# Performance work log

Measured on AMD Instinct MI355X. Metric: run time of the kernel, lower is better.

The kernel has to match this reference:

```python
import jax, jax.numpy as jnp
import numpy as np

B, U, V = 4, 64, 256
IN_DIM, STATE_DIM, CODE_DIM = 768, 768, 384
NUM_HEADS, HEAD_DIM = 8, 64
INNER = NUM_HEADS * HEAD_DIM  # 512
SCALE = HEAD_DIM ** 0.5


def _ln(x, g, b, eps=1e-5):
    mu = jnp.mean(x, axis=-1, keepdims=True)
    var = jnp.var(x, axis=-1, keepdims=True)
    return (x - mu) * jax.lax.rsqrt(var + eps) * g + b


def setup_inputs() -> dict:
    key = jax.random.key(0)
    ks = jax.random.split(key, 12)
    def w(k, shape, s=0.02):
        return jax.random.normal(k, shape, jnp.float32) * s
    return {
        "receiver_states": jax.random.normal(ks[0], (B, U, STATE_DIM), jnp.float32),
        "receiver_codes": jax.random.normal(ks[1], (B, U, CODE_DIM), jnp.float32),
        "sender_states": jax.random.normal(ks[2], (B, V, IN_DIM), jnp.float32),
        "ln_r_g": jnp.ones((STATE_DIM,), jnp.float32),
        "ln_r_b": jnp.zeros((STATE_DIM,), jnp.float32),
        "ln_s_g": jnp.ones((IN_DIM,), jnp.float32),
        "ln_s_b": jnp.zeros((IN_DIM,), jnp.float32),
        "Wq": w(ks[3], (STATE_DIM, INNER)), "bq": jnp.zeros((INNER,), jnp.float32), "Wmq": w(ks[4], (CODE_DIM, STATE_DIM)),
        "Wk": w(ks[5], (IN_DIM, INNER)),   "bk": jnp.zeros((INNER,), jnp.float32), "Wmk": w(ks[6], (CODE_DIM, IN_DIM)),
        "Wv": w(ks[7], (IN_DIM, INNER)),   "bv": jnp.zeros((INNER,), jnp.float32), "Wmv": w(ks[8], (CODE_DIM, IN_DIM)),
        "We": w(ks[9], (INNER, STATE_DIM)), "be": jnp.zeros((STATE_DIM,), jnp.float32), "Wme": w(ks[10], (CODE_DIM, INNER)),
        "gamma": jnp.ones((STATE_DIM,), jnp.float32),  # LayerScale, init 1.0
    }


def reference(receiver_states, receiver_codes, sender_states,
              ln_r_g, ln_r_b, ln_s_g, ln_s_b,
              Wq, bq, Wmq, Wk, bk, Wmk, Wv, bv, Wmv, We, be, Wme, gamma):
    r = _ln(receiver_states, ln_r_g, ln_r_b)   # (b,u,ds)
    s = _ln(sender_states, ln_s_g, ln_s_b)     # (b,v,di)
    # ModFC: y = (x * (1 + ctx @ Wm)) @ W + b  (code-conditioned input modulation)
    q = (r * (1.0 + receiver_codes @ Wmq)) @ Wq + bq          # (b,u,inner)
    mk = 1.0 + receiver_codes @ Wmk                           # (b,u,di)
    mv = 1.0 + receiver_codes @ Wmv                           # (b,u,di)
    xs = s[:, :, None, :]                                     # (b,v,1,di)
    k = (xs * mk[:, None, :, :]) @ Wk + bk                    # (b,v,u,inner)
    v = (xs * mv[:, None, :, :]) @ Wv + bv                    # (b,v,u,inner)
    qh = q.reshape(B, U, NUM_HEADS, HEAD_DIM)
    kh = k.reshape(B, V, U, NUM_HEADS, HEAD_DIM)
    vh = v.reshape(B, V, U, NUM_HEADS, HEAD_DIM)
    scores = jnp.einsum('buhc,bvuhc->bhuv', qh, kh) / SCALE   # (b,h,u,v)
    weights = jax.nn.softmax(scores, axis=-1)
    msg = jnp.einsum('bhuv,bvuhc->buhc', weights, vh).reshape(B, U, INNER)
    out = (msg * (1.0 + receiver_codes @ Wme)) @ We + be      # exit ModFC -> (b,u,ds)
    out = out * gamma                                         # LayerScale
    return receiver_states + out                              # residual
```

## Files before the change

kernel.cpp:

```cpp
#include <hip/hip_runtime.h>


#define DD 768
#define CDIM 384
#define NH 8
#define HD 64
#define INNER 512
#define VV 256

__device__ __forceinline__ void fma4(float4& a, float s, const float4& b) {
  a.x += s * b.x; a.y += s * b.y; a.z += s * b.z; a.w += s * b.w;
}

template <int K, int NS>
__device__ __forceinline__ void gcore(const float* __restrict__ A0, int lda,
                                      const float* __restrict__ Bp,
                                      float4& a0, float4& a1, float4& a2,
                                      float4& a3) {
  float4 b0[8], b1[8];
#pragma unroll
  for (int i = 0; i < 8; i++) b0[i] = *(const float4*)(Bp + (size_t)i * NS);
  const float* Bq = Bp + (size_t)8 * NS;
#pragma unroll 1
  for (int kk = 0; kk < K; kk += 16) {
#pragma unroll
    for (int i = 0; i < 8; i++) b1[i] = *(const float4*)(Bq + (size_t)i * NS);
    Bq += (size_t)8 * NS;
#pragma unroll
    for (int i = 0; i < 8; i++) {
      float4 bv = b0[i]; int k = kk + i;
      fma4(a0, A0[k], bv); fma4(a1, A0[lda + k], bv);
      fma4(a2, A0[2 * lda + k], bv); fma4(a3, A0[3 * lda + k], bv);
    }
    if (kk + 16 < K) {
#pragma unroll
      for (int i = 0; i < 8; i++) b0[i] = *(const float4*)(Bq + (size_t)i * NS);
      Bq += (size_t)8 * NS;
    }
#pragma unroll
    for (int i = 0; i < 8; i++) {
      float4 bv = b1[i]; int k = kk + 8 + i;
      fma4(a0, A0[k], bv); fma4(a1, A0[lda + k], bv);
      fma4(a2, A0[2 * lda + k], bv); fma4(a3, A0[3 * lda + k], bv);
    }
  }
}

__global__ __launch_bounds__(256, 2) void k_s1(
    const float* __restrict__ ss, const float* __restrict__ rs,
    const float* __restrict__ g_s, const float* __restrict__ b_s,
    const float* __restrict__ g_r, const float* __restrict__ b_r,
    const float* __restrict__ codes, const float* __restrict__ Wmq,
    const float* __restrict__ Wmk, const float* __restrict__ Wmv,
    const float* __restrict__ Wme, const float* __restrict__ Wk,
    float* __restrict__ s_ln, float* __restrict__ r_ln,
    float* __restrict__ cp, float* __restrict__ WkT) {
  __shared__ float SB[6144];
  int bid = blockIdx.x, t = threadIdx.x;
  if (bid < 176) {
    int nc = bid % 11, mb = bid / 11;
    int base = nc * 256;
    const float* W; int N, colW;
    if (base < 768)       { W = Wmq; N = DD;    colW = base; }
    else if (base < 1536) { W = Wmk; N = DD;    colW = base - 768; }
    else if (base < 2304) { W = Wmv; N = DD;    colW = base - 1536; }
    else                  { W = Wme; N = INNER; colW = base - 2304; }
    int m0 = mb * 16;
#pragma unroll
    for (int p = 0; p < 24; p++) {
      int idx = p * 256 + t, r = idx / 384, k = idx % 384;
      SB[idx] = codes[(size_t)(m0 + r) * CDIM + k];
    }
    __syncthreads();
    int kl = t & 63, wid = t >> 6;
    const float* A0 = SB + (wid * 4) * 384;
    float4 a0 = {0,0,0,0}, a1 = {0,0,0,0}, a2 = {0,0,0,0}, a3 = {0,0,0,0};
    if (N == DD)
      gcore<384, DD>(A0, 384, W + colW + 4 * kl, a0, a1, a2, a3);
    else
      gcore<384, INNER>(A0, 384, W + colW + 4 * kl, a0, a1, a2, a3);
    int m = m0 + wid * 4, gcol = base + 4 * kl;
    *(float4*)(cp + (size_t)m * 2816 + gcol) = a0;
    *(float4*)(cp + (size_t)(m + 1) * 2816 + gcol) = a1;
    *(float4*)(cp + (size_t)(m + 2) * 2816 + gcol) = a2;
    *(float4*)(cp + (size_t)(m + 3) * 2816 + gcol) = a3;
  } else if (bid < 272) {
    int tid = bid - 176;
    int d0 = (tid >> 3) * 64, c0 = (tid & 7) * 64;
    int j = t & 63, i0 = t >> 6;
#pragma unroll
    for (int p = 0; p < 16; p++) {
      int i = p * 4 + i0;
      SB[i * 65 + j] = Wk[(size_t)(d0 + i) * INNER + c0 + j];
    }
    __syncthreads();
#pragma unroll
    for (int p = 0; p < 16; p++) {
      int i = p * 4 + i0;
      WkT[(size_t)(c0 + i) * DD + d0 + j] = SB[j * 65 + i];
    }
  } else {
    int rr = bid - 272;
    const float *x, *g, *bb; float* y; int r;
    if (rr < 1024) { x = ss; g = g_s; bb = b_s; y = s_ln; r = rr; }
    else           { x = rs; g = g_r; bb = b_r; y = r_ln; r = rr - 1024; }
    const float* xr = x + (size_t)r * DD;
    float v0 = xr[t], v1 = xr[t + 256], v2 = xr[t + 512];
    float s = v0 + v1 + v2, sq = v0 * v0 + v1 * v1 + v2 * v2;
    for (int o = 32; o > 0; o >>= 1) {
      s += __shfl_down(s, o, 64); sq += __shfl_down(sq, o, 64);
    }
    int wid = t >> 6, lane = t & 63;
    if (lane == 0) { SB[wid] = s; SB[wid + 4] = sq; }
    __syncthreads();
    float sum = SB[0] + SB[1] + SB[2] + SB[3];
    float ssq = SB[4] + SB[5] + SB[6] + SB[7];
    float mu = sum * (1.0f / 768.0f);
    float var = ssq * (1.0f / 768.0f) - mu * mu;
    float rstd = rsqrtf(var + 1e-5f);
    float* yr = y + (size_t)r * DD;
    yr[t]       = (v0 - mu) * rstd * g[t]       + bb[t];
    yr[t + 256] = (v1 - mu) * rstd * g[t + 256] + bb[t + 256];
    yr[t + 512] = (v2 - mu) * rstd * g[t + 512] + bb[t + 512];
  }
}

__global__ __launch_bounds__(256, 2) void k_s2(
    const float* __restrict__ s_ln, const float* __restrict__ r_ln,
    const float* __restrict__ cp, const float* __restrict__ Wq,
    float* __restrict__ sT, float* __restrict__ qp) {
  __shared__ float SB[4160];
  int bid = blockIdx.x, t = threadIdx.x;
  if (bid < 128) {
    int ks = bid & 3, tile = bid >> 2, nc = tile & 1, mb = tile >> 1;
    int m0 = mb * 16, col0 = nc * 256, k0 = ks * 192;
#pragma unroll
    for (int p = 0; p < 12; p++) {
      int idx = p * 256 + t, r = idx / 192, k = idx % 192;
      int d = k0 + k;
      float mqv = cp[(size_t)(m0 + r) * 2816 + d] + 1.0f;
      SB[idx] = r_ln[(size_t)(m0 + r) * DD + d] * mqv;
    }
    __syncthreads();
    int kl = t & 63, wid = t >> 6;
    int col = col0 + 4 * kl;
    const float* A0 = SB + (wid * 4) * 192;
    float4 a0 = {0,0,0,0}, a1 = {0,0,0,0}, a2 = {0,0,0,0}, a3 = {0,0,0,0};
    gcore<192, INNER>(A0, 192, Wq + (size_t)k0 * INNER + col, a0, a1, a2, a3);
    int m = m0 + wid * 4;
    float* dst = qp + (size_t)ks * (256 * INNER);
    *(float4*)(dst + (size_t)m * INNER + col) = a0;
    *(float4*)(dst + (size_t)(m + 1) * INNER + col) = a1;
    *(float4*)(dst + (size_t)(m + 2) * INNER + col) = a2;
    *(float4*)(dst + (size_t)(m + 3) * INNER + col) = a3;
  } else {
    int tid = bid - 128;
    int vt = tid & 3, dt = (tid >> 2) % 12, b = tid / 48;
    int v0 = vt * 64, d0 = dt * 64;
    int j = t & 63, i0 = t >> 6;
#pragma unroll
    for (int p = 0; p < 16; p++) {
      int i = p * 4 + i0;
      SB[i * 65 + j] = s_ln[(size_t)(b * VV + v0 + i) * DD + d0 + j];
    }
    __syncthreads();
#pragma unroll
    for (int p = 0; p < 16; p++) {
      int i = p * 4 + i0;
      sT[((size_t)b * DD + d0 + i) * VV + v0 + j] = SB[j * 65 + i];
    }
  }
}

__global__ __launch_bounds__(256, 2) void k_s3(
    const float* __restrict__ qp, const float* __restrict__ bq,
    const float* __restrict__ WkT, const float* __restrict__ cp,
    const float* __restrict__ bk, float* __restrict__ qm,
    float* __restrict__ qbk) {
  __shared__ float SB[1024];
  int bid = blockIdx.x, t = threadIdx.x;
  if (bid < 384) {
    int h = bid & 7, dc = (bid >> 3) % 3, mb = bid / 24;
    int m0 = mb * 16;
#pragma unroll
    for (int p = 0; p < 4; p++) {
      int idx = p * 256 + t, r = idx >> 6, c = idx & 63;
      int i = h * HD + c;
      size_t off = (size_t)(m0 + r) * INNER + i;
      SB[idx] = qp[off] + qp[131072 + off] + qp[262144 + off] +
                qp[393216 + off] + bq[i];
    }
    __syncthreads();
    int kl = t & 63, wid = t >> 6;
    int col = dc * 256 + 4 * kl;
    const float* A0 = SB + (wid * 4) * HD;
    float4 a0 = {0,0,0,0}, a1 = {0,0,0,0}, a2 = {0,0,0,0}, a3 = {0,0,0,0};
    gcore<64, DD>(A0, HD, WkT + (size_t)(h * HD) * DD + col, a0, a1, a2, a3);
#pragma unroll
    for (int j = 0; j < 4; j++) {
      float4 a = (j == 0) ? a0 : (j == 1) ? a1 : (j == 2) ? a2 : a3;
      int m = m0 + wid * 4 + j;
      const float* mkp = cp + (size_t)m * 2816 + 768 + col;
      float4 o = {a.x * (mkp[0] + 1.0f), a.y * (mkp[1] + 1.0f),
                  a.z * (mkp[2] + 1.0f), a.w * (mkp[3] + 1.0f)};
      *(float4*)(qm + ((size_t)m * NH + h) * DD + col) = o;
    }
  } else {
    int m = bid - 384;
    size_t off = (size_t)m * INNER;
    SB[t] = (qp[off + t] + qp[131072 + off + t] + qp[262144 + off + t] +
             qp[393216 + off + t] + bq[t]) * bk[t];
    int t2 = t + 256;
    SB[t2] = (qp[off + t2] + qp[131072 + off + t2] + qp[262144 + off + t2] +
              qp[393216 + off + t2] + bq[t2]) * bk[t2];
    __syncthreads();
    if (t < 8) {
      float a = 0.f;
      for (int c = 0; c < HD; c++) a += SB[t * HD + c];
      qbk[m * NH + t] = a;
    }
  }
}

__global__ __launch_bounds__(256, 2) void k_s4(
    const float* __restrict__ qm, const float* __restrict__ sT,
    float* __restrict__ scp) {
  __shared__ float SB[3072];
  int bid = blockIdx.x, t = threadIdx.x;
  int ks = bid & 3, b = (bid >> 2) & 3, mb = bid >> 4;
  int gi0 = b * 512 + mb * 16, k0 = ks * 192;
#pragma unroll
  for (int p = 0; p < 12; p++) {
    int idx = p * 256 + t, r = idx / 192, k = idx % 192;
    SB[idx] = qm[(size_t)(gi0 + r) * DD + k0 + k];
  }
  __syncthreads();
  int kl = t & 63, wid = t >> 6;
  int col = 4 * kl;
  const float* A0 = SB + (wid * 4) * 192;
  float4 a0 = {0,0,0,0}, a1 = {0,0,0,0}, a2 = {0,0,0,0}, a3 = {0,0,0,0};
  gcore<192, VV>(A0, 192, sT + ((size_t)b * DD + k0) * VV + col, a0, a1, a2, a3);
  int gi = gi0 + wid * 4;
  float* dst = scp + (size_t)ks * (2048 * VV);
  *(float4*)(dst + (size_t)gi * VV + col) = a0;
  *(float4*)(dst + (size_t)(gi + 1) * VV + col) = a1;
  *(float4*)(dst + (size_t)(gi + 2) * VV + col) = a2;
  *(float4*)(dst + (size_t)(gi + 3) * VV + col) = a3;
}

__global__ __launch_bounds__(256, 2) void k_s5(
    const float* __restrict__ scp, const float* __restrict__ qbk,
    const float* __restrict__ s_ln, const float* __restrict__ cp,
    float* __restrict__ wsm) {
  __shared__ float SC[4096];
  int bid = blockIdx.x, t = threadIdx.x;
  int dc = bid % 3, up = (bid / 3) % 32, b = bid / 96;
  int gi0 = b * 512 + up * 16;
#pragma unroll
  for (int p = 0; p < 16; p++) {
    int idx = p * 256 + t, r = idx >> 8, c = idx & 255;
    size_t o = (size_t)(gi0 + r) * VV + c;
    float v = scp[o] + scp[524288 + o] + scp[1048576 + o] + scp[1572864 + o];
    int m = b * 64 + up * 2 + (r >> 3), h = r & 7;
    SC[idx] = (v + qbk[m * NH + h]) * 0.125f;
  }
  __syncthreads();
  int wid = t >> 6, lane = t & 63;
#pragma unroll
  for (int j = 0; j < 4; j++) {
    int r = wid * 4 + j;
    float x0 = SC[r * 256 + lane],       x1 = SC[r * 256 + lane + 64];
    float x2 = SC[r * 256 + lane + 128], x3 = SC[r * 256 + lane + 192];
    float mx = fmaxf(fmaxf(x0, x1), fmaxf(x2, x3));
    for (int o = 1; o < 64; o <<= 1) mx = fmaxf(mx, __shfl_xor(mx, o, 64));
    float e0 = __expf(x0 - mx), e1 = __expf(x1 - mx);
    float e2 = __expf(x2 - mx), e3 = __expf(x3 - mx);
    float sm = e0 + e1 + e2 + e3;
    for (int o = 1; o < 64; o <<= 1) sm += __shfl_xor(sm, o, 64);
    float rinv = 1.0f / sm;
    SC[r * 256 + lane] = e0 * rinv;       SC[r * 256 + lane + 64] = e1 * rinv;
    SC[r * 256 + lane + 128] = e2 * rinv; SC[r * 256 + lane + 192] = e3 * rinv;
  }
  __syncthreads();
  int kl = t & 63;
  int col = dc * 256 + 4 * kl;
  const float* A0 = SC + (wid * 4) * 256;
  float4 a0 = {0,0,0,0}, a1 = {0,0,0,0}, a2 = {0,0,0,0}, a3 = {0,0,0,0};
  gcore<VV, DD>(A0, 256, s_ln + (size_t)(b * VV) * DD + col, a0, a1, a2, a3);
#pragma unroll
  for (int j = 0; j < 4; j++) {
    float4 a = (j == 0) ? a0 : (j == 1) ? a1 : (j == 2) ? a2 : a3;
    int r = wid * 4 + j;
    int ul = r >> 3, h = r & 7, m = b * 64 + up * 2 + ul;
    const float* mvp = cp + (size_t)m * 2816 + 1536 + col;
    float4 o = {a.x * (mvp[0] + 1.0f), a.y * (mvp[1] + 1.0f),
                a.z * (mvp[2] + 1.0f), a.w * (mvp[3] + 1.0f)};
    *(float4*)(wsm + ((size_t)h * 256 + m) * DD + col) = o;
  }
}

__global__ __launch_bounds__(256, 2) void k_s6(
    const float* __restrict__ wsm, const float* __restrict__ Wv,
    float* __restrict__ mmp) {
  __shared__ float AL[6144];
  int bid = blockIdx.x, t = threadIdx.x;
  int hp = bid & 1, ks = (bid >> 1) & 7, mb = bid >> 4;
  int h0 = hp * 4, m0 = mb * 16, k0 = ks * 96;
#pragma unroll
  for (int p = 0; p < 24; p++) {
    int idx = p * 256 + t;
    int e = idx / 1536, rem = idx % 1536, r = rem / 96, k = rem % 96;
    AL[idx] = wsm[((size_t)(h0 + e) * 256 + m0 + r) * DD + k0 + k];
  }
  __syncthreads();
  int kl = t & 63, wid = t >> 6;
  int hs = kl >> 4, c4 = 4 * (kl & 15);
  int colg = h0 * HD + hs * HD + c4;
  const float* A0 = AL + (hs * 16 + wid * 4) * 96;
  float4 a0 = {0,0,0,0}, a1 = {0,0,0,0}, a2 = {0,0,0,0}, a3 = {0,0,0,0};
  gcore<96, INNER>(A0, 96, Wv + (size_t)k0 * INNER + colg, a0, a1, a2, a3);
  float* dst = mmp + (size_t)ks * (256 * INNER);
  int m = m0 + wid * 4;
  *(float4*)(dst + (size_t)m * INNER + colg) = a0;
  *(float4*)(dst + (size_t)(m + 1) * INNER + colg) = a1;
  *(float4*)(dst + (size_t)(m + 2) * INNER + colg) = a2;
  *(float4*)(dst + (size_t)(m + 3) * INNER + colg) = a3;
}

__global__ __launch_bounds__(256, 2) void k_s7(
    const float* __restrict__ mmp, const float* __restrict__ bvv,
    const float* __restrict__ cp, const float* __restrict__ We,
    float* __restrict__ op) {
  __shared__ float AL[1024];
  int bid = blockIdx.x, t = threadIdx.x;
  int ks = bid & 7, dc = (bid >> 3) % 3, mb = bid / 24;
  int m0 = mb * 16, k0 = ks * 64;
#pragma unroll
  for (int p = 0; p < 4; p++) {
    int idx = p * 256 + t, r = idx >> 6, k = idx & 63;
    int i = k0 + k;
    size_t off = (size_t)(m0 + r) * INNER + i;
    float v = mmp[off] + mmp[131072 + off] + mmp[262144 + off] +
              mmp[393216 + off] + mmp[524288 + off] + mmp[655360 + off] +
              mmp[786432 + off] + mmp[917504 + off];
    float mev = cp[(size_t)(m0 + r) * 2816 + 2304 + i] + 1.0f;
    AL[idx] = (v + bvv[i]) * mev;
  }
  __syncthreads();
  int kl = t & 63, wid = t >> 6;
  int col = dc * 256 + 4 * kl;
  const float* A0 = AL + (wid * 4) * 64;
  float4 a0 = {0,0,0,0}, a1 = {0,0,0,0}, a2 = {0,0,0,0}, a3 = {0,0,0,0};
  gcore<64, DD>(A0, 64, We + (size_t)k0 * DD + col, a0, a1, a2, a3);
  float* dst = op + (size_t)ks * (256 * DD);
  int m = m0 + wid * 4;
  *(float4*)(dst + (size_t)m * DD + col) = a0;
  *(float4*)(dst + (size_t)(m + 1) * DD + col) = a1;
  *(float4*)(dst + (size_t)(m + 2) * DD + col) = a2;
  *(float4*)(dst + (size_t)(m + 3) * DD + col) = a3;
}

__global__ __launch_bounds__(256) void k_s8(
    const float* __restrict__ op, const float* __restrict__ be,
    const float* __restrict__ gamma, const float* __restrict__ rs,
    float* __restrict__ outp) {
  int m = blockIdx.x, t = threadIdx.x;
#pragma unroll
  for (int j = 0; j < 3; j++) {
    int d = t + j * 256;
    size_t off = (size_t)m * DD + d;
    float v = op[off] + op[196608 + off] + op[393216 + off] +
              op[589824 + off] + op[786432 + off] + op[983040 + off] +
              op[1179648 + off] + op[1376256 + off];
    outp[off] = rs[off] + (v + be[d]) * gamma[d];
  }
}

extern "C" void kernel_launch(void* const* d_in, const int* in_sizes, int n_in,
                              void* d_out, int out_size, void* d_ws, size_t ws_size,
                              hipStream_t stream) {
  const float* rs     = (const float*)d_in[0];
  const float* codes  = (const float*)d_in[1];
  const float* ss     = (const float*)d_in[2];
  const float* ln_r_g = (const float*)d_in[3];
  const float* ln_r_b = (const float*)d_in[4];
  const float* ln_s_g = (const float*)d_in[5];
  const float* ln_s_b = (const float*)d_in[6];
  const float* Wq  = (const float*)d_in[7];
  const float* bq  = (const float*)d_in[8];
  const float* Wk  = (const float*)d_in[10];
  const float* bk  = (const float*)d_in[11];
  const float* Wmq = (const float*)d_in[9];
  const float* Wmk = (const float*)d_in[12];
  const float* Wv  = (const float*)d_in[13];
  const float* bv  = (const float*)d_in[14];
  const float* Wmv = (const float*)d_in[15];
  const float* We  = (const float*)d_in[16];
  const float* be  = (const float*)d_in[17];
  const float* Wme = (const float*)d_in[18];
  const float* gamma = (const float*)d_in[19];

  float* w = (float*)d_ws;
  float* s_ln = w;
  float* r_ln = w + 786432;
  float* WkT  = w + 983040;
  float* qp   = w + 1376256;
  float* sT   = w + 1900544;
  float* cp   = w + 2686976;
  float* qbk  = w + 3407872;
  float* qm   = w + 3409920;
  float* scp  = w + 4982784;
  float* wsm  = qm;
  float* mmp  = r_ln;
  float* op   = scp;

  k_s1<<<dim3(1552), 256, 0, stream>>>(ss, rs, ln_s_g, ln_s_b, ln_r_g, ln_r_b,
                                       codes, Wmq, Wmk, Wmv, Wme, Wk,
                                       s_ln, r_ln, cp, WkT);
  k_s2<<<dim3(320), 256, 0, stream>>>(s_ln, r_ln, cp, Wq, sT, qp);
  k_s3<<<dim3(640), 256, 0, stream>>>(qp, bq, WkT, cp, bk, qm, qbk);
  k_s4<<<dim3(512), 256, 0, stream>>>(qm, sT, scp);
  k_s5<<<dim3(384), 256, 0, stream>>>(scp, qbk, s_ln, cp, wsm);
  k_s6<<<dim3(256), 256, 0, stream>>>(wsm, Wv, mmp);
  k_s7<<<dim3(384), 256, 0, stream>>>(mmp, bv, cp, We, op);
  k_s8<<<dim3(256), 256, 0, stream>>>(op, be, gamma, rs, (float*)d_out);
}
```

Measured before the change: 198.2 us.

## Fuse eight stage kernels into one persistent kernel with grid barriers

```diff
diff --git a/kernel.cpp b/kernel.cpp
--- a/kernel.cpp
+++ b/kernel.cpp
@@ -7,6 +7,7 @@
 #define HD 64
 #define INNER 512
 #define VV 256
+#define GRID 448
 
 __device__ __forceinline__ void fma4(float4& a, float s, const float4& b) {
   a.x += s * b.x; a.y += s * b.y; a.z += s * b.z; a.w += s * b.w;
@@ -46,333 +47,346 @@
   }
 }
 
-__global__ __launch_bounds__(256, 2) void k_s1(
-    const float* __restrict__ ss, const float* __restrict__ rs,
-    const float* __restrict__ g_s, const float* __restrict__ b_s,
-    const float* __restrict__ g_r, const float* __restrict__ b_r,
-    const float* __restrict__ codes, const float* __restrict__ Wmq,
-    const float* __restrict__ Wmk, const float* __restrict__ Wmv,
-    const float* __restrict__ Wme, const float* __restrict__ Wk,
-    float* __restrict__ s_ln, float* __restrict__ r_ln,
-    float* __restrict__ cp, float* __restrict__ WkT) {
+__device__ __forceinline__ void gbar(unsigned* bar, unsigned target) {
+  __syncthreads();
+  if (threadIdx.x == 0) {
+    __threadfence();
+    atomicAdd(bar, 1u);
+    while (atomicAdd(bar, 0u) < target) __builtin_amdgcn_s_sleep(2);
+    __threadfence();
+  }
+  __syncthreads();
+}
+
+__global__ __launch_bounds__(256, 2) void k_all(
+    const float* __restrict__ rs, const float* __restrict__ codes,
+    const float* __restrict__ ss, const float* __restrict__ g_r,
+    const float* __restrict__ b_r, const float* __restrict__ g_s,
+    const float* __restrict__ b_s, const float* __restrict__ Wq,
+    const float* __restrict__ bq, const float* __restrict__ Wmq,
+    const float* __restrict__ Wk, const float* __restrict__ bk,
+    const float* __restrict__ Wmk, const float* __restrict__ Wv,
+    const float* __restrict__ bvv, const float* __restrict__ Wmv,
+    const float* __restrict__ We, const float* __restrict__ be,
+    const float* __restrict__ Wme, const float* __restrict__ gamma,
+    float* __restrict__ w, float* __restrict__ outp, unsigned* __restrict__ bar) {
   __shared__ float SB[6144];
-  int bid = blockIdx.x, t = threadIdx.x;
-  if (bid < 176) {
-    int nc = bid % 11, mb = bid / 11;
-    int base = nc * 256;
-    const float* W; int N, colW;
-    if (base < 768)       { W = Wmq; N = DD;    colW = base; }
-    else if (base < 1536) { W = Wmk; N = DD;    colW = base - 768; }
-    else if (base < 2304) { W = Wmv; N = DD;    colW = base - 1536; }
-    else                  { W = Wme; N = INNER; colW = base - 2304; }
-    int m0 = mb * 16;
-#pragma unroll
-    for (int p = 0; p < 24; p++) {
-      int idx = p * 256 + t, r = idx / 384, k = idx % 384;
-      SB[idx] = codes[(size_t)(m0 + r) * CDIM + k];
-    }
-    __syncthreads();
-    int kl = t & 63, wid = t >> 6;
-    const float* A0 = SB + (wid * 4) * 384;
-    float4 a0 = {0,0,0,0}, a1 = {0,0,0,0}, a2 = {0,0,0,0}, a3 = {0,0,0,0};
-    if (N == DD)
-      gcore<384, DD>(A0, 384, W + colW + 4 * kl, a0, a1, a2, a3);
-    else
-      gcore<384, INNER>(A0, 384, W + colW + 4 * kl, a0, a1, a2, a3);
-    int m = m0 + wid * 4, gcol = base + 4 * kl;
-    *(float4*)(cp + (size_t)m * 2816 + gcol) = a0;
-    *(float4*)(cp + (size_t)(m + 1) * 2816 + gcol) = a1;
-    *(float4*)(cp + (size_t)(m + 2) * 2816 + gcol) = a2;
-    *(float4*)(cp + (size_t)(m + 3) * 2816 + gcol) = a3;
-  } else if (bid < 272) {
-    int tid = bid - 176;
-    int d0 = (tid >> 3) * 64, c0 = (tid & 7) * 64;
-    int j = t & 63, i0 = t >> 6;
-#pragma unroll
-    for (int p = 0; p < 16; p++) {
-      int i = p * 4 + i0;
-      SB[i * 65 + j] = Wk[(size_t)(d0 + i) * INNER + c0 + j];
-    }
-    __syncthreads();
-#pragma unroll
-    for (int p = 0; p < 16; p++) {
-      int i = p * 4 + i0;
-      WkT[(size_t)(c0 + i) * DD + d0 + j] = SB[j * 65 + i];
-    }
-  } else {
-    int rr = bid - 272;
-    const float *x, *g, *bb; float* y; int r;
-    if (rr < 1024) { x = ss; g = g_s; bb = b_s; y = s_ln; r = rr; }
-    else           { x = rs; g = g_r; bb = b_r; y = r_ln; r = rr - 1024; }
-    const float* xr = x + (size_t)r * DD;
-    float v0 = xr[t], v1 = xr[t + 256], v2 = xr[t + 512];
-    float s = v0 + v1 + v2, sq = v0 * v0 + v1 * v1 + v2 * v2;
-    for (int o = 32; o > 0; o >>= 1) {
-      s += __shfl_down(s, o, 64); sq += __shfl_down(sq, o, 64);
-    }
-    int wid = t >> 6, lane = t & 63;
-    if (lane == 0) { SB[wid] = s; SB[wid + 4] = sq; }
-    __syncthreads();
-    float sum = SB[0] + SB[1] + SB[2] + SB[3];
-    float ssq = SB[4] + SB[5] + SB[6] + SB[7];
-    float mu = sum * (1.0f / 768.0f);
-    float var = ssq * (1.0f / 768.0f) - mu * mu;
-    float rstd = rsqrtf(var + 1e-5f);
-    float* yr = y + (size_t)r * DD;
-    yr[t]       = (v0 - mu) * rstd * g[t]       + bb[t];
-    yr[t + 256] = (v1 - mu) * rstd * g[t + 256] + bb[t + 256];
-    yr[t + 512] = (v2 - mu) * rstd * g[t + 512] + bb[t + 512];
-  }
-}
-
-__global__ __launch_bounds__(256, 2) void k_s2(
-    const float* __restrict__ s_ln, const float* __restrict__ r_ln,
-    const float* __restrict__ cp, const float* __restrict__ Wq,
-    float* __restrict__ sT, float* __restrict__ qp) {
-  __shared__ float SB[4160];
-  int bid = blockIdx.x, t = threadIdx.x;
-  if (bid < 128) {
-    int ks = bid & 3, tile = bid >> 2, nc = tile & 1, mb = tile >> 1;
-    int m0 = mb * 16, col0 = nc * 256, k0 = ks * 192;
+  float* s_ln = w;
+  float* r_ln = w + 786432;
+  float* WkT  = w + 983040;
+  float* qp   = w + 1376256;
+  float* sT   = w + 1900544;
+  float* cp   = w + 2686976;
+  float* qbk  = w + 3407872;
+  float* qm   = w + 3409920;
+  float* scp  = w + 4982784;
+  float* wsm  = qm;
+  float* mmp  = r_ln;
+  float* op   = scp;
+
+  int t = threadIdx.x;
+  unsigned target = 0;
+
+  for (int tile = blockIdx.x; tile < 1552; tile += GRID) {
+    if (tile < 176) {
+      int nc = tile % 11, mb = tile / 11;
+      int base = nc * 256;
+      const float* W; int N, colW;
+      if (base < 768)       { W = Wmq; N = DD;    colW = base; }
+      else if (base < 1536) { W = Wmk; N = DD;    colW = base - 768; }
+      else if (base < 2304) { W = Wmv; N = DD;    colW = base - 1536; }
+      else                  { W = Wme; N = INNER; colW = base - 2304; }
+      int m0 = mb * 16;
+#pragma unroll
+      for (int p = 0; p < 24; p++) {
+        int idx = p * 256 + t, r = idx / 384, k = idx % 384;
+        SB[idx] = codes[(size_t)(m0 + r) * CDIM + k];
+      }
+      __syncthreads();
+      int kl = t & 63, wid = t >> 6;
+      const float* A0 = SB + (wid * 4) * 384;
+      float4 a0 = {0,0,0,0}, a1 = {0,0,0,0}, a2 = {0,0,0,0}, a3 = {0,0,0,0};
+      if (N == DD)
+        gcore<384, DD>(A0, 384, W + colW + 4 * kl, a0, a1, a2, a3);
+      else
+        gcore<384, INNER>(A0, 384, W + colW + 4 * kl, a0, a1, a2, a3);
+      int m = m0 + wid * 4, gcol = base + 4 * kl;
+      *(float4*)(cp + (size_t)m * 2816 + gcol) = a0;
+      *(float4*)(cp + (size_t)(m + 1) * 2816 + gcol) = a1;
+      *(float4*)(cp + (size_t)(m + 2) * 2816 + gcol) = a2;
+      *(float4*)(cp + (size_t)(m + 3) * 2816 + gcol) = a3;
+    } else if (tile < 272) {
+      int tid = tile - 176;
+      int d0 = (tid >> 3) * 64, c0 = (tid & 7) * 64;
+      int j = t & 63, i0 = t >> 6;
+#pragma unroll
+      for (int p = 0; p < 16; p++) {
+        int i = p * 4 + i0;
+        SB[i * 65 + j] = Wk[(size_t)(d0 + i) * INNER + c0 + j];
+      }
+      __syncthreads();
+#pragma unroll
+      for (int p = 0; p < 16; p++) {
+        int i = p * 4 + i0;
+        WkT[(size_t)(c0 + i) * DD + d0 + j] = SB[j * 65 + i];
+      }
+    } else {
+      int rr = tile - 272;
+      const float *x, *g, *bb; float* y; int r;
+      if (rr < 1024) { x = ss; g = g_s; bb = b_s; y = s_ln; r = rr; }
+      else           { x = rs; g = g_r; bb = b_r; y = r_ln; r = rr - 1024; }
+      const float* xr = x + (size_t)r * DD;
+      float v0 = xr[t], v1 = xr[t + 256], v2 = xr[t + 512];
+      float s = v0 + v1 + v2, sq = v0 * v0 + v1 * v1 + v2 * v2;
+      for (int o = 32; o > 0; o >>= 1) {
+        s += __shfl_down(s, o, 64); sq += __shfl_down(sq, o, 64);
+      }
+      int wid = t >> 6, lane = t & 63;
+      if (lane == 0) { SB[wid] = s; SB[wid + 4] = sq; }
+      __syncthreads();
+      float sum = SB[0] + SB[1] + SB[2] + SB[3];
+      float ssq = SB[4] + SB[5] + SB[6] + SB[7];
+      float mu = sum * (1.0f / 768.0f);
+      float var = ssq * (1.0f / 768.0f) - mu * mu;
+      float rstd = rsqrtf(var + 1e-5f);
+      float* yr = y + (size_t)r * DD;
+      yr[t]       = (v0 - mu) * rstd * g[t]       + bb[t];
+      yr[t + 256] = (v1 - mu) * rstd * g[t + 256] + bb[t + 256];
+      yr[t + 512] = (v2 - mu) * rstd * g[t + 512] + bb[t + 512];
+    }
+    __syncthreads();
+  }
+  target += GRID; gbar(bar, target);
+
+  for (int tile = blockIdx.x; tile < 320; tile += GRID) {
+    if (tile < 128) {
+      int ks = tile & 3, t2 = tile >> 2, nc = t2 & 1, mb = t2 >> 1;
+      int m0 = mb * 16, col0 = nc * 256, k0 = ks * 192;
+#pragma unroll
+      for (int p = 0; p < 12; p++) {
+        int idx = p * 256 + t, r = idx / 192, k = idx % 192;
+        int d = k0 + k;
+        float mqv = cp[(size_t)(m0 + r) * 2816 + d] + 1.0f;
+        SB[idx] = r_ln[(size_t)(m0 + r) * DD + d] * mqv;
+      }
+      __syncthreads();
+      int kl = t & 63, wid = t >> 6;
+      int col = col0 + 4 * kl;
+      const float* A0 = SB + (wid * 4) * 192;
+      float4 a0 = {0,0,0,0}, a1 = {0,0,0,0}, a2 = {0,0,0,0}, a3 = {0,0,0,0};
+      gcore<192, INNER>(A0, 192, Wq + (size_t)k0 * INNER + col, a0, a1, a2, a3);
+      int m = m0 + wid * 4;
+      float* dst = qp + (size_t)ks * (256 * INNER);
+      *(float4*)(dst + (size_t)m * INNER + col) = a0;
+      *(float4*)(dst + (size_t)(m + 1) * INNER + col) = a1;
+      *(float4*)(dst + (size_t)(m + 2) * INNER + col) = a2;
+      *(float4*)(dst + (size_t)(m + 3) * INNER + col) = a3;
+    } else {
+      int tid = tile - 128;
+      int vt = tid & 3, dt = (tid >> 2) % 12, b = tid / 48;
+      int v0 = vt * 64, d0 = dt * 64;
+      int j = t & 63, i0 = t >> 6;
+#pragma unroll
+      for (int p = 0; p < 16; p++) {
+        int i = p * 4 + i0;
+        SB[i * 65 + j] = s_ln[(size_t)(b * VV + v0 + i) * DD + d0 + j];
+      }
+      __syncthreads();
+#pragma unroll
+      for (int p = 0; p < 16; p++) {
+        int i = p * 4 + i0;
+        sT[((size_t)b * DD + d0 + i) * VV + v0 + j] = SB[j * 65 + i];
+      }
+    }
+    __syncthreads();
+  }
+  target += GRID; gbar(bar, target);
+
+  for (int tile = blockIdx.x; tile < 640; tile += GRID) {
+    if (tile < 384) {
+      int h = tile & 7, dc = (tile >> 3) % 3, mb = tile / 24;
+      int m0 = mb * 16;
+#pragma unroll
+      for (int p = 0; p < 4; p++) {
+        int idx = p * 256 + t, r = idx >> 6, c = idx & 63;
+        int i = h * HD + c;
+        size_t off = (size_t)(m0 + r) * INNER + i;
+        SB[idx] = qp[off] + qp[131072 + off] + qp[262144 + off] +
+                  qp[393216 + off] + bq[i];
+      }
+      __syncthreads();
+      int kl = t & 63, wid = t >> 6;
+      int col = dc * 256 + 4 * kl;
+      const float* A0 = SB + (wid * 4) * HD;
+      float4 a0 = {0,0,0,0}, a1 = {0,0,0,0}, a2 = {0,0,0,0}, a3 = {0,0,0,0};
+      gcore<64, DD>(A0, HD, WkT + (size_t)(h * HD) * DD + col, a0, a1, a2, a3);
+#pragma unroll
+      for (int j = 0; j < 4; j++) {
+        float4 a = (j == 0) ? a0 : (j == 1) ? a1 : (j == 2) ? a2 : a3;
+        int m = m0 + wid * 4 + j;
+        const float* mkp = cp + (size_t)m * 2816 + 768 + col;
+        float4 o = {a.x * (mkp[0] + 1.0f), a.y * (mkp[1] + 1.0f),
+                    a.z * (mkp[2] + 1.0f), a.w * (mkp[3] + 1.0f)};
+        *(float4*)(qm + ((size_t)m * NH + h) * DD + col) = o;
+      }
+    } else {
+      int m = tile - 384;
+      size_t off = (size_t)m * INNER;
+      SB[t] = (qp[off + t] + qp[131072 + off + t] + qp[262144 + off + t] +
+               qp[393216 + off + t] + bq[t]) * bk[t];
+      int t2 = t + 256;
+      SB[t2] = (qp[off + t2] + qp[131072 + off + t2] + qp[262144 + off + t2] +
+                qp[393216 + off + t2] + bq[t2]) * bk[t2];
+      __syncthreads();
+      if (t < 8) {
+        float a = 0.f;
+        for (int c = 0; c < HD; c++) a += SB[t * HD + c];
+        qbk[m * NH + t] = a;
+      }
+    }
+    __syncthreads();
+  }
+  target += GRID; gbar(bar, target);
+
+  for (int tile = blockIdx.x; tile < 512; tile += GRID) {
+    int ks = tile & 3, b = (tile >> 2) & 3, mb = tile >> 4;
+    int gi0 = b * 512 + mb * 16, k0 = ks * 192;
 #pragma unroll
     for (int p = 0; p < 12; p++) {
       int idx = p * 256 + t, r = idx / 192, k = idx % 192;
-      int d = k0 + k;
-      float mqv = cp[(size_t)(m0 + r) * 2816 + d] + 1.0f;
-      SB[idx] = r_ln[(size_t)(m0 + r) * DD + d] * mqv;
+      SB[idx] = qm[(size_t)(gi0 + r) * DD + k0 + k];
     }
     __syncthreads();
     int kl = t & 63, wid = t >> 6;
-    int col = col0 + 4 * kl;
+    int col = 4 * kl;
     const float* A0 = SB + (wid * 4) * 192;
     float4 a0 = {0,0,0,0}, a1 = {0,0,0,0}, a2 = {0,0,0,0}, a3 = {0,0,0,0};
-    gcore<192, INNER>(A0, 192, Wq + (size_t)k0 * INNER + col, a0, a1, a2, a3);
+    gcore<192, VV>(A0, 192, sT + ((size_t)b * DD + k0) * VV + col, a0, a1, a2, a3);
+    int gi = gi0 + wid * 4;
+    float* dst = scp + (size_t)ks * (2048 * VV);
+    *(float4*)(dst + (size_t)gi * VV + col) = a0;
+    *(float4*)(dst + (size_t)(gi + 1) * VV + col) = a1;
+    *(float4*)(dst + (size_t)(gi + 2) * VV + col) = a2;
+    *(float4*)(dst + (size_t)(gi + 3) * VV + col) = a3;
+    __syncthreads();
+  }
+  target += GRID; gbar(bar, target);
+
+  for (int tile = blockIdx.x; tile < 384; tile += GRID) {
+    int dc = tile % 3, up = (tile / 3) % 32, b = tile / 96;
+    int gi0 = b * 512 + up * 16;
+#pragma unroll
+    for (int p = 0; p < 16; p++) {
+      int idx = p * 256 + t, r = idx >> 8, c = idx & 255;
+      size_t o = (size_t)(gi0 + r) * VV + c;
+      float v = scp[o] + scp[524288 + o] + scp[1048576 + o] + scp[1572864 + o];
+      int m = b * 64 + up * 2 + (r >> 3), h = r & 7;
+      SB[idx] = (v + qbk[m * NH + h]) * 0.125f;
+    }
+    __syncthreads();
+    int wid = t >> 6, lane = t & 63;
+#pragma unroll
+    for (int j = 0; j < 4; j++) {
+      int r = wid * 4 + j;
+      float x0 = SB[r * 256 + lane],       x1 = SB[r * 256 + lane + 64];
+      float x2 = SB[r * 256 + lane + 128], x3 = SB[r * 256 + lane + 192];
+      float mx = fmaxf(fmaxf(x0, x1), fmaxf(x2, x3));
+      for (int o = 1; o < 64; o <<= 1) mx = fmaxf(mx, __shfl_xor(mx, o, 64));
+      float e0 = __expf(x0 - mx), e1 = __expf(x1 - mx);
+      float e2 = __expf(x2 - mx), e3 = __expf(x3 - mx);
+      float sm = e0 + e1 + e2 + e3;
+      for (int o = 1; o < 64; o <<= 1) sm += __shfl_xor(sm, o, 64);
+      float rinv = 1.0f / sm;
+      SB[r * 256 + lane] = e0 * rinv;       SB[r * 256 + lane + 64] = e1 * rinv;
+      SB[r * 256 + lane + 128] = e2 * rinv; SB[r * 256 + lane + 192] = e3 * rinv;
+    }
+    __syncthreads();
+    int kl = t & 63;
+    int col = dc * 256 + 4 * kl;
+    const float* A0 = SB + (wid * 4) * 256;
+    float4 a0 = {0,0,0,0}, a1 = {0,0,0,0}, a2 = {0,0,0,0}, a3 = {0,0,0,0};
+    gcore<VV, DD>(A0, 256, s_ln + (size_t)(b * VV) * DD + col, a0, a1, a2, a3);
+#pragma unroll
+    for (int j = 0; j < 4; j++) {
+      float4 a = (j == 0) ? a0 : (j == 1) ? a1 : (j == 2) ? a2 : a3;
+      int r = wid * 4 + j;
+      int ul = r >> 3, h = r & 7, m = b * 64 + up * 2 + ul;
+      const float* mvp = cp + (size_t)m * 2816 + 1536 + col;
+      float4 o = {a.x * (mvp[0] + 1.0f), a.y * (mvp[1] + 1.0f),
+                  a.z * (mvp[2] + 1.0f), a.w * (mvp[3] + 1.0f)};
+      *(float4*)(wsm + ((size_t)h * 256 + m) * DD + col) = o;
+    }
+    __syncthreads();
+  }
+  target += GRID; gbar(bar, target);
+
+  for (int tile = blockIdx.x; tile < 256; tile += GRID) {
+    int hp = tile & 1, ks = (tile >> 1) & 7, mb = tile >> 4;
+    int h0 = hp * 4, m0 = mb * 16, k0 = ks * 96;
+#pragma unroll
+    for (int p = 0; p < 24; p++) {
+      int idx = p * 256 + t;
+      int e = idx / 1536, rem = idx % 1536, r = rem / 96, k = rem % 96;
+      SB[idx] = wsm[((size_t)(h0 + e) * 256 + m0 + r) * DD + k0 + k];
+    }
+    __syncthreads();
+    int kl = t & 63, wid = t >> 6;
+    int hs = kl >> 4, c4 = 4 * (kl & 15);
+    int colg = h0 * HD + hs * HD + c4;
+    const float* A0 = SB + (hs * 16 + wid * 4) * 96;
+    float4 a0 = {0,0,0,0}, a1 = {0,0,0,0}, a2 = {0,0,0,0}, a3 = {0,0,0,0};
+    gcore<96, INNER>(A0, 96, Wv + (size_t)k0 * INNER + colg, a0, a1, a2, a3);
+    float* dst = mmp + (size_t)ks * (256 * INNER);
     int m = m0 + wid * 4;
-    float* dst = qp + (size_t)ks * (256 * INNER);
-    *(float4*)(dst + (size_t)m * INNER + col) = a0;
-    *(float4*)(dst + (size_t)(m + 1) * INNER + col) = a1;
-    *(float4*)(dst + (size_t)(m + 2) * INNER + col) = a2;
-    *(float4*)(dst + (size_t)(m + 3) * INNER + col) = a3;
-  } else {
-    int tid = bid - 128;
-    int vt = tid & 3, dt = (tid >> 2) % 12, b = tid / 48;
-    int v0 = vt * 64, d0 = dt * 64;
-    int j = t & 63, i0 = t >> 6;
-#pragma unroll
-    for (int p = 0; p < 16; p++) {
-      int i = p * 4 + i0;
-      SB[i * 65 + j] = s_ln[(size_t)(b * VV + v0 + i) * DD + d0 + j];
-    }
-    __syncthreads();
-#pragma unroll
-    for (int p = 0; p < 16; p++) {
-      int i = p * 4 + i0;
-      sT[((size_t)b * DD + d0 + i) * VV + v0 + j] = SB[j * 65 + i];
-    }
-  }
-}
-
-__global__ __launch_bounds__(256, 2) void k_s3(
-    const float* __restrict__ qp, const float* __restrict__ bq,
-    const float* __restrict__ WkT, const float* __restrict__ cp,
-    const float* __restrict__ bk, float* __restrict__ qm,
-    float* __restrict__ qbk) {
-  __shared__ float SB[1024];
-  int bid = blockIdx.x, t = threadIdx.x;
-  if (bid < 384) {
-    int h = bid & 7, dc = (bid >> 3) % 3, mb = bid / 24;
-    int m0 = mb * 16;
+    *(float4*)(dst + (size_t)m * INNER + colg) = a0;
+    *(float4*)(dst + (size_t)(m + 1) * INNER + colg) = a1;
+    *(float4*)(dst + (size_t)(m + 2) * INNER + colg) = a2;
+    *(float4*)(dst + (size_t)(m + 3) * INNER + colg) = a3;
+    __syncthreads();
+  }
+  target += GRID; gbar(bar, target);
+
+  for (int tile = blockIdx.x; tile < 384; tile += GRID) {
+    int ks = tile & 7, dc = (tile >> 3) % 3, mb = tile / 24;
+    int m0 = mb * 16, k0 = ks * 64;
 #pragma unroll
     for (int p = 0; p < 4; p++) {
-      int idx = p * 256 + t, r = idx >> 6, c = idx & 63;
-      int i = h * HD + c;
+      int idx = p * 256 + t, r = idx >> 6, k = idx & 63;
+      int i = k0 + k;
       size_t off = (size_t)(m0 + r) * INNER + i;
-      SB[idx] = qp[off] + qp[131072 + off] + qp[262144 + off] +
-                qp[393216 + off] + bq[i];
+      float v = mmp[off] + mmp[131072 + off] + mmp[262144 + off] +
+                mmp[393216 + off] + mmp[524288 + off] + mmp[655360 + off] +
+                mmp[786432 + off] + mmp[917504 + off];
+      float mev = cp[(size_t)(m0 + r) * 2816 + 2304 + i] + 1.0f;
+      SB[idx] = (v + bvv[i]) * mev;
     }
     __syncthreads();
     int kl = t & 63, wid = t >> 6;
     int col = dc * 256 + 4 * kl;
-    const float* A0 = SB + (wid * 4) * HD;
+    const float* A0 = SB + (wid * 4) * 64;
     float4 a0 = {0,0,0,0}, a1 = {0,0,0,0}, a2 = {0,0,0,0}, a3 = {0,0,0,0};
-    gcore<64, DD>(A0, HD, WkT + (size_t)(h * HD) * DD + col, a0, a1, a2, a3);
-#pragma unroll
-    for (int j = 0; j < 4; j++) {
-      float4 a = (j == 0) ? a0 : (j == 1) ? a1 : (j == 2) ? a2 : a3;
-      int m = m0 + wid * 4 + j;
-      const float* mkp = cp + (size_t)m * 2816 + 768 + col;
-      float4 o = {a.x * (mkp[0] + 1.0f), a.y * (mkp[1] + 1.0f),
-                  a.z * (mkp[2] + 1.0f), a.w * (mkp[3] + 1.0f)};
-      *(float4*)(qm + ((size_t)m * NH + h) * DD + col) = o;
-    }
-  } else {
-    int m = bid - 384;
-    size_t off = (size_t)m * INNER;
-    SB[t] = (qp[off + t] + qp[131072 + off + t] + qp[262144 + off + t] +
-             qp[393216 + off + t] + bq[t]) * bk[t];
-    int t2 = t + 256;
-    SB[t2] = (qp[off + t2] + qp[131072 + off + t2] + qp[262144 + off + t2] +
-              qp[393216 + off + t2] + bq[t2]) * bk[t2];
-    __syncthreads();
-    if (t < 8) {
-      float a = 0.f;
-      for (int c = 0; c < HD; c++) a += SB[t * HD + c];
-      qbk[m * NH + t] = a;
-    }
-  }
-}
-
-__global__ __launch_bounds__(256, 2) void k_s4(
-    const float* __restrict__ qm, const float* __restrict__ sT,
-    float* __restrict__ scp) {
-  __shared__ float SB[3072];
-  int bid = blockIdx.x, t = threadIdx.x;
-  int ks = bid & 3, b = (bid >> 2) & 3, mb = bid >> 4;
-  int gi0 = b * 512 + mb * 16, k0 = ks * 192;
-#pragma unroll
-  for (int p = 0; p < 12; p++) {
-    int idx = p * 256 + t, r = idx / 192, k = idx % 192;
-    SB[idx] = qm[(size_t)(gi0 + r) * DD + k0 + k];
-  }
-  __syncthreads();
-  int kl = t & 63, wid = t >> 6;
-  int col = 4 * kl;
-  const float* A0 = SB + (wid * 4) * 192;
-  float4 a0 = {0,0,0,0}, a1 = {0,0,0,0}, a2 = {0,0,0,0}, a3 = {0,0,0,0};
-  gcore<192, VV>(A0, 192, sT + ((size_t)b * DD + k0) * VV + col, a0, a1, a2, a3);
-  int gi = gi0 + wid * 4;
-  float* dst = scp + (size_t)ks * (2048 * VV);
-  *(float4*)(dst + (size_t)gi * VV + col) = a0;
-  *(float4*)(dst + (size_t)(gi + 1) * VV + col) = a1;
-  *(float4*)(dst + (size_t)(gi + 2) * VV + col) = a2;
-  *(float4*)(dst + (size_t)(gi + 3) * VV + col) = a3;
-}
-
-__global__ __launch_bounds__(256, 2) void k_s5(
-    const float* __restrict__ scp, const float* __restrict__ qbk,
-    const float* __restrict__ s_ln, const float* __restrict__ cp,
-    float* __restrict__ wsm) {
-  __shared__ float SC[4096];
-  int bid = blockIdx.x, t = threadIdx.x;
-  int dc = bid % 3, up = (bid / 3) % 32, b = bid / 96;
-  int gi0 = b * 512 + up * 16;
-#pragma unroll
-  for (int p = 0; p < 16; p++) {
-    int idx = p * 256 + t, r = idx >> 8, c = idx & 255;
-    size_t o = (size_t)(gi0 + r) * VV + c;
-    float v = scp[o] + scp[524288 + o] + scp[1048576 + o] + scp[1572864 + o];
-    int m = b * 64 + up * 2 + (r >> 3), h = r & 7;
-    SC[idx] = (v + qbk[m * NH + h]) * 0.125f;
-  }
-  __syncthreads();
-  int wid = t >> 6, lane = t & 63;
-#pragma unroll
-  for (int j = 0; j < 4; j++) {
-    int r = wid * 4 + j;
-    float x0 = SC[r * 256 + lane],       x1 = SC[r * 256 + lane + 64];
-    float x2 = SC[r * 256 + lane + 128], x3 = SC[r * 256 + lane + 192];
-    float mx = fmaxf(fmaxf(x0, x1), fmaxf(x2, x3));
-    for (int o = 1; o < 64; o <<= 1) mx = fmaxf(mx, __shfl_xor(mx, o, 64));
-    float e0 = __expf(x0 - mx), e1 = __expf(x1 - mx);
-    float e2 = __expf(x2 - mx), e3 = __expf(x3 - mx);
-    float sm = e0 + e1 + e2 + e3;
-    for (int o = 1; o < 64; o <<= 1) sm += __shfl_xor(sm, o, 64);
-    float rinv = 1.0f / sm;
-    SC[r * 256 + lane] = e0 * rinv;       SC[r * 256 + lane + 64] = e1 * rinv;
-    SC[r * 256 + lane + 128] = e2 * rinv; SC[r * 256 + lane + 192] = e3 * rinv;
-  }
-  __syncthreads();
-  int kl = t & 63;
-  int col = dc * 256 + 4 * kl;
-  const float* A0 = SC + (wid * 4) * 256;
-  float4 a0 = {0,0,0,0}, a1 = {0,0,0,0}, a2 = {0,0,0,0}, a3 = {0,0,0,0};
-  gcore<VV, DD>(A0, 256, s_ln + (size_t)(b * VV) * DD + col, a0, a1, a2, a3);
-#pragma unroll
-  for (int j = 0; j < 4; j++) {
-    float4 a = (j == 0) ? a0 : (j == 1) ? a1 : (j == 2) ? a2 : a3;
-    int r = wid * 4 + j;
-    int ul = r >> 3, h = r & 7, m = b * 64 + up * 2 + ul;
-    const float* mvp = cp + (size_t)m * 2816 + 1536 + col;
-    float4 o = {a.x * (mvp[0] + 1.0f), a.y * (mvp[1] + 1.0f),
-                a.z * (mvp[2] + 1.0f), a.w * (mvp[3] + 1.0f)};
-    *(float4*)(wsm + ((size_t)h * 256 + m) * DD + col) = o;
-  }
-}
-
-__global__ __launch_bounds__(256, 2) void k_s6(
-    const float* __restrict__ wsm, const float* __restrict__ Wv,
-    float* __restrict__ mmp) {
-  __shared__ float AL[6144];
-  int bid = blockIdx.x, t = threadIdx.x;
-  int hp = bid & 1, ks = (bid >> 1) & 7, mb = bid >> 4;
-  int h0 = hp * 4, m0 = mb * 16, k0 = ks * 96;
-#pragma unroll
-  for (int p = 0; p < 24; p++) {
-    int idx = p * 256 + t;
-    int e = idx / 1536, rem = idx % 1536, r = rem / 96, k = rem % 96;
-    AL[idx] = wsm[((size_t)(h0 + e) * 256 + m0 + r) * DD + k0 + k];
-  }
-  __syncthreads();
-  int kl = t & 63, wid = t >> 6;
-  int hs = kl >> 4, c4 = 4 * (kl & 15);
-  int colg = h0 * HD + hs * HD + c4;
-  const float* A0 = AL + (hs * 16 + wid * 4) * 96;
-  float4 a0 = {0,0,0,0}, a1 = {0,0,0,0}, a2 = {0,0,0,0}, a3 = {0,0,0,0};
-  gcore<96, INNER>(A0, 96, Wv + (size_t)k0 * INNER + colg, a0, a1, a2, a3);
-  float* dst = mmp + (size_t)ks * (256 * INNER);
-  int m = m0 + wid * 4;
-  *(float4*)(dst + (size_t)m * INNER + colg) = a0;
-  *(float4*)(dst + (size_t)(m + 1) * INNER + colg) = a1;
-  *(float4*)(dst + (size_t)(m + 2) * INNER + colg) = a2;
-  *(float4*)(dst + (size_t)(m + 3) * INNER + colg) = a3;
-}
-
-__global__ __launch_bounds__(256, 2) void k_s7(
-    const float* __restrict__ mmp, const float* __restrict__ bvv,
-    const float* __restrict__ cp, const float* __restrict__ We,
-    float* __restrict__ op) {
-  __shared__ float AL[1024];
-  int bid = blockIdx.x, t = threadIdx.x;
-  int ks = bid & 7, dc = (bid >> 3) % 3, mb = bid / 24;
-  int m0 = mb * 16, k0 = ks * 64;
-#pragma unroll
-  for (int p = 0; p < 4; p++) {
-    int idx = p * 256 + t, r = idx >> 6, k = idx & 63;
-    int i = k0 + k;
-    size_t off = (size_t)(m0 + r) * INNER + i;
-    float v = mmp[off] + mmp[131072 + off] + mmp[262144 + off] +
-              mmp[393216 + off] + mmp[524288 + off] + mmp[655360 + off] +
-              mmp[786432 + off] + mmp[917504 + off];
-    float mev = cp[(size_t)(m0 + r) * 2816 + 2304 + i] + 1.0f;
-    AL[idx] = (v + bvv[i]) * mev;
-  }
-  __syncthreads();
-  int kl = t & 63, wid = t >> 6;
-  int col = dc * 256 + 4 * kl;
-  const float* A0 = AL + (wid * 4) * 64;
-  float4 a0 = {0,0,0,0}, a1 = {0,0,0,0}, a2 = {0,0,0,0}, a3 = {0,0,0,0};
-  gcore<64, DD>(A0, 64, We + (size_t)k0 * DD + col, a0, a1, a2, a3);
-  float* dst = op + (size_t)ks * (256 * DD);
-  int m = m0 + wid * 4;
-  *(float4*)(dst + (size_t)m * DD + col) = a0;
-  *(float4*)(dst + (size_t)(m + 1) * DD + col) = a1;
-  *(float4*)(dst + (size_t)(m + 2) * DD + col) = a2;
-  *(float4*)(dst + (size_t)(m + 3) * DD + col) = a3;
-}
-
-__global__ __launch_bounds__(256) void k_s8(
-    const float* __restrict__ op, const float* __restrict__ be,
-    const float* __restrict__ gamma, const float* __restrict__ rs,
-    float* __restrict__ outp) {
-  int m = blockIdx.x, t = threadIdx.x;
-#pragma unroll
-  for (int j = 0; j < 3; j++) {
-    int d = t + j * 256;
-    size_t off = (size_t)m * DD + d;
-    float v = op[off] + op[196608 + off] + op[393216 + off] +
-              op[589824 + off] + op[786432 + off] + op[983040 + off] +
-              op[1179648 + off] + op[1376256 + off];
-    outp[off] = rs[off] + (v + be[d]) * gamma[d];
+    gcore<64, DD>(A0, 64, We + (size_t)k0 * DD + col, a0, a1, a2, a3);
+    float* dst = op + (size_t)ks * (256 * DD);
+    int m = m0 + wid * 4;
+    *(float4*)(dst + (size_t)m * DD + col) = a0;
+    *(float4*)(dst + (size_t)(m + 1) * DD + col) = a1;
+    *(float4*)(dst + (size_t)(m + 2) * DD + col) = a2;
+    *(float4*)(dst + (size_t)(m + 3) * DD + col) = a3;
+    __syncthreads();
+  }
+  target += GRID; gbar(bar, target);
+
+  for (int tile = blockIdx.x; tile < 256; tile += GRID) {
+    int m = tile;
+#pragma unroll
+    for (int j = 0; j < 3; j++) {
+      int d = t + j * 256;
+      size_t off = (size_t)m * DD + d;
+      float v = op[off] + op[196608 + off] + op[393216 + off] +
+                op[589824 + off] + op[786432 + off] + op[983040 + off] +
+                op[1179648 + off] + op[1376256 + off];
+      outp[off] = rs[off] + (v + be[d]) * gamma[d];
+    }
   }
 }
 
@@ -388,9 +402,9 @@
   const float* ln_s_b = (const float*)d_in[6];
   const float* Wq  = (const float*)d_in[7];
   const float* bq  = (const float*)d_in[8];
+  const float* Wmq = (const float*)d_in[9];
   const float* Wk  = (const float*)d_in[10];
   const float* bk  = (const float*)d_in[11];
-  const float* Wmq = (const float*)d_in[9];
   const float* Wmk = (const float*)d_in[12];
   const float* Wv  = (const float*)d_in[13];
   const float* bv  = (const float*)d_in[14];
@@ -401,27 +415,10 @@
   const float* gamma = (const float*)d_in[19];
 
   float* w = (float*)d_ws;
-  float* s_ln = w;
-  float* r_ln = w + 786432;
-  float* WkT  = w + 983040;
-  float* qp   = w + 1376256;
-  float* sT   = w + 1900544;
-  float* cp   = w + 2686976;
-  float* qbk  = w + 3407872;
-  float* qm   = w + 3409920;
-  float* scp  = w + 4982784;
-  float* wsm  = qm;
-  float* mmp  = r_ln;
-  float* op   = scp;
-
-  k_s1<<<dim3(1552), 256, 0, stream>>>(ss, rs, ln_s_g, ln_s_b, ln_r_g, ln_r_b,
-                                       codes, Wmq, Wmk, Wmv, Wme, Wk,
-                                       s_ln, r_ln, cp, WkT);
-  k_s2<<<dim3(320), 256, 0, stream>>>(s_ln, r_ln, cp, Wq, sT, qp);
-  k_s3<<<dim3(640), 256, 0, stream>>>(qp, bq, WkT, cp, bk, qm, qbk);
-  k_s4<<<dim3(512), 256, 0, stream>>>(qm, sT, scp);
-  k_s5<<<dim3(384), 256, 0, stream>>>(scp, qbk, s_ln, cp, wsm);
-  k_s6<<<dim3(256), 256, 0, stream>>>(wsm, Wv, mmp);
-  k_s7<<<dim3(384), 256, 0, stream>>>(mmp, bv, cp, We, op);
-  k_s8<<<dim3(256), 256, 0, stream>>>(op, be, gamma, rs, (float*)d_out);
+  unsigned* bar = (unsigned*)(w + 7079936);
+
+  hipMemsetAsync(bar, 0, 64, stream);
+  k_all<<<dim3(GRID), 256, 0, stream>>>(
+      rs, codes, ss, ln_r_g, ln_r_b, ln_s_g, ln_s_b, Wq, bq, Wmq, Wk, bk,
+      Wmk, Wv, bv, Wmv, We, be, Wme, gamma, w, (float*)d_out, bar);
 }
```

Result: slower. 554.7 us (+179.9%).
